# Performance work log

Hardware: AMD Instinct MI355X
Metric: run time of the kernel (lower is better)

The kernel has to match this reference:

```python
import jax, jax.numpy as jnp
import numpy as np

N, IN, HID, OUT = 8192, 512, 256, 128

def setup_inputs() -> dict:
    key = jax.random.key(0)
    k1, k2, k3, k4 = jax.random.split(key, 4)
    adj = jax.random.uniform(k1, (N, N), dtype=jnp.float32)
    feature = jax.random.normal(k2, (N, IN), dtype=jnp.float32)
    W1 = jax.random.normal(k3, (IN, HID), dtype=jnp.float32) * (1.0 / np.sqrt(IN))
    b1 = jnp.zeros((HID,), dtype=jnp.float32)
    W2 = jax.random.normal(k4, (HID, OUT), dtype=jnp.float32) * (1.0 / np.sqrt(HID))
    b2 = jnp.zeros((OUT,), dtype=jnp.float32)
    return {"adj": adj, "feature": feature, "W1": W1, "b1": b1, "W2": W2, "b2": b2}

def reference(adj, feature, W1, b1, W2, b2):
    # GCN encoder: layer1 (relu) then layer2 (linear output)
    h = jax.nn.relu(adj @ (feature @ W1) + b1)   # [N, HID]
    h = adj @ (h @ W2) + b2                      # [N, OUT]
    # InnerProductDecoder: sigmoid(flatten(h @ h.T))
    logits = h @ h.T                             # [N, N]
    h_noise = jax.nn.sigmoid(logits.reshape(-1)) # [N*N]
    return (h_noise, h)
```

## Files before the change

### kernel.cpp

```cpp
#include <hip/hip_runtime.h>


typedef __bf16 bf16x8_t __attribute__((ext_vector_type(8)));
typedef __bf16 bf16x4_t __attribute__((ext_vector_type(4)));
typedef float  f32x4_t  __attribute__((ext_vector_type(4)));

#define MFMA_BF16(a, b, c) __builtin_amdgcn_mfma_f32_16x16x32_bf16((a), (b), (c), 0, 0, 0)

__device__ __forceinline__ bf16x8_t cvt8(float4 u, float4 v) {
    bf16x8_t o;
    o[0] = (__bf16)u.x; o[1] = (__bf16)u.y; o[2] = (__bf16)u.z; o[3] = (__bf16)u.w;
    o[4] = (__bf16)v.x; o[5] = (__bf16)v.y; o[6] = (__bf16)v.z; o[7] = (__bf16)v.w;
    return o;
}

template<int AUX>
__device__ __forceinline__ void gload_lds16(const float* g, float* l) {
    __builtin_amdgcn_global_load_lds(
        (const __attribute__((address_space(1))) unsigned int*)g,
        (__attribute__((address_space(3))) unsigned int*)l, 16, 0, AUX);
}

__global__ __launch_bounds__(256) void cast_all(
    const float* __restrict__ feat, const float* __restrict__ W1,
    const float* __restrict__ W2, __bf16* __restrict__ fb,
    __bf16* __restrict__ w1t, __bf16* __restrict__ w2t)
{
    const int j = blockIdx.x * 256 + threadIdx.x;
    if (j < 524288) {
        const float4* p = (const float4*)feat + (size_t)j * 2;
        float4 u = p[0], v = p[1];
        *(bf16x8_t*)(fb + (size_t)j * 8) = cvt8(u, v);
    } else if (j < 524288 + 131072) {
        int t = j - 524288;
        int k = t >> 8, n = t & 255;
        w1t[n * 512 + k] = (__bf16)W1[t];
    } else if (j < 524288 + 131072 + 32768) {
        int t = j - 655360;
        int k = t >> 7, n = t & 127;
        w2t[n * 256 + k] = (__bf16)W2[t];
    }
}

template<int MT, int WC>
__global__ __launch_bounds__(256, 2) void gemm_bt_cbf16(
    const __bf16* __restrict__ X, const __bf16* __restrict__ Yb,
    __bf16* __restrict__ C, int K, int N)
{
    constexpr int WR = 4 / WC;
    constexpr int BM = WR * MT * 16;
    constexpr int BN = WC * 64;
    const int mblk = blockIdx.x, nblk = blockIdx.y;
    const int w = threadIdx.x >> 6, lane = threadIdx.x & 63;
    const int wr = w / WC, wc = w % WC;
    const int q = lane >> 4, l16 = lane & 15;
    const int mbase = mblk * BM + wr * (MT * 16);
    const int nbase = nblk * BN + wc * 64;

    f32x4_t acc[MT][4];
    const f32x4_t z = {0.f, 0.f, 0.f, 0.f};
#pragma unroll
    for (int i = 0; i < MT; i++)
#pragma unroll
        for (int jj = 0; jj < 4; jj++) acc[i][jj] = z;

    const __bf16* Xr[MT];
    const __bf16* Yr[4];
#pragma unroll
    for (int i = 0; i < MT; i++) Xr[i] = X + (size_t)(mbase + i * 16 + l16) * K + q * 8;
#pragma unroll
    for (int jj = 0; jj < 4; jj++) Yr[jj] = Yb + (size_t)(nbase + jj * 16 + l16) * K + q * 8;

    for (int k = 0; k < K; k += 32) {
        bf16x8_t a[MT], b[4];
#pragma unroll
        for (int i = 0; i < MT; i++) a[i] = *(const bf16x8_t*)(Xr[i] + k);
#pragma unroll
        for (int jj = 0; jj < 4; jj++) b[jj] = *(const bf16x8_t*)(Yr[jj] + k);
#pragma unroll
        for (int i = 0; i < MT; i++)
#pragma unroll
            for (int jj = 0; jj < 4; jj++) acc[i][jj] = MFMA_BF16(a[i], b[jj], acc[i][jj]);
    }

#pragma unroll
    for (int i = 0; i < MT; i++)
#pragma unroll
        for (int jj = 0; jj < 4; jj++) {
            const int row0 = mbase + i * 16 + q * 4;
            const int col = nbase + jj * 16 + l16;
#pragma unroll
            for (int r = 0; r < 4; r++)
                C[(size_t)(row0 + r) * N + col] = (__bf16)acc[i][jj][r];
        }
}

template<int NN>
__global__ __launch_bounds__(256, 2) void gemm_adj_lds(
    const float* __restrict__ A, const __bf16* __restrict__ Y,
    float* __restrict__ P, int kchunk)
{
    constexpr int NT = NN / 64;
    __shared__ float As[2][4096];

    const int mblk = blockIdx.x;
    const int ks = blockIdx.y;
    const int w = threadIdx.x >> 6, lane = threadIdx.x & 63;
    const int q = lane >> 4, l16 = lane & 15;
    const int kbase = ks * kchunk;
    const int ntiles = kchunk >> 6;

    const int lrow = lane >> 4;
    const int lg = lane & 15;
    const float* gsrc[4];
    int loff[4];
#pragma unroll
    for (int j = 0; j < 4; j++) {
        const int row = j * 16 + w * 4 + lrow;
        const int colswz = ((lg ^ (row & 15)) << 2);
        gsrc[j] = A + (size_t)(mblk * 64 + row) * 8192 + kbase + colswz;
        loff[j] = row * 64 + (lg << 2);
    }

    const __bf16* Yr[NT];
#pragma unroll
    for (int jj = 0; jj < NT; jj++)
        Yr[jj] = Y + (size_t)(w * (NN / 4) + jj * 16 + l16) * 8192 + q * 8;

    f32x4_t acc[4][NT];
    const f32x4_t z = {0.f, 0.f, 0.f, 0.f};
#pragma unroll
    for (int i = 0; i < 4; i++)
#pragma unroll
        for (int jj = 0; jj < NT; jj++) acc[i][jj] = z;

#pragma unroll
    for (int j = 0; j < 4; j++) gload_lds16<2>(gsrc[j], &As[0][0] + loff[j]);

    int buf = 0;
    for (int kt = 0; kt < ntiles; kt++) {
        const int kk = kbase + (kt << 6);

        bf16x8_t breg[2][NT];
#pragma unroll
        for (int s = 0; s < 2; s++)
#pragma unroll
            for (int jj = 0; jj < NT; jj++)
                breg[s][jj] = *(const bf16x8_t*)(Yr[jj] + kk + s * 32);

        __syncthreads();

        if (kt + 1 < ntiles) {
            const int koff = (kt + 1) << 6;
#pragma unroll
            for (int j = 0; j < 4; j++)
                gload_lds16<2>(gsrc[j] + koff, &As[buf ^ 1][0] + loff[j]);
        }

        const float* __restrict__ L = &As[buf][0];
#pragma unroll
        for (int s = 0; s < 2; s++) {
            bf16x8_t a[4];
#pragma unroll
            for (int i = 0; i < 4; i++) {
                const int r = i * 16 + l16;
                const int g0 = ((s * 8 + q * 2) ^ l16) << 2;
                const int g1 = ((s * 8 + q * 2 + 1) ^ l16) << 2;
                float4 u = *(const float4*)(L + r * 64 + g0);
                float4 v = *(const float4*)(L + r * 64 + g1);
                a[i] = cvt8(u, v);
            }
#pragma unroll
            for (int i = 0; i < 4; i++)
#pragma unroll
                for (int jj = 0; jj < NT; jj++)
                    acc[i][jj] = MFMA_BF16(a[i], breg[s][jj], acc[i][jj]);
        }
        buf ^= 1;
    }

#pragma unroll
    for (int i = 0; i < 4; i++)
#pragma unroll
        for (int jj = 0; jj < NT; jj++) {
            const int row0 = mblk * 64 + i * 16 + q * 4;
            const int col = w * (NN / 4) + jj * 16 + l16;
            float* pp = P + ((size_t)ks * 8192 + row0) * NN + col;
#pragma unroll
            for (int r = 0; r < 4; r++) pp[(size_t)r * NN] = acc[i][jj][r];
        }
}

__global__ __launch_bounds__(256) void epi_relu_bias(
    const float* __restrict__ P, const float* __restrict__ bias,
    __bf16* __restrict__ H)
{
    const size_t SL = (size_t)8192 * 256;
    const size_t idx = ((size_t)blockIdx.x * 256 + threadIdx.x) * 4;
    float4 s0 = *(const float4*)(P + idx);
    float4 s1 = *(const float4*)(P + SL + idx);
    float4 s2 = *(const float4*)(P + 2 * SL + idx);
    float4 s3 = *(const float4*)(P + 3 * SL + idx);
    const int col = (int)(idx & 255);
    float4 bb = *(const float4*)(bias + col);
    float r0 = fmaxf(s0.x + s1.x + s2.x + s3.x + bb.x, 0.f);
    float r1 = fmaxf(s0.y + s1.y + s2.y + s3.y + bb.y, 0.f);
    float r2 = fmaxf(s0.z + s1.z + s2.z + s3.z + bb.z, 0.f);
    float r3 = fmaxf(s0.w + s1.w + s2.w + s3.w + bb.w, 0.f);
    bf16x4_t o;
    o[0] = (__bf16)r0; o[1] = (__bf16)r1; o[2] = (__bf16)r2; o[3] = (__bf16)r3;
    *(bf16x4_t*)(H + idx) = o;
}

__global__ __launch_bounds__(256) void epi_bias_out(
    const float* __restrict__ P, const float* __restrict__ bias,
    float* __restrict__ Hout, __bf16* __restrict__ Hbf)
{
    const size_t SL = (size_t)8192 * 128;
    const size_t idx = ((size_t)blockIdx.x * 256 + threadIdx.x) * 4;
    float4 s0 = *(const float4*)(P + idx);
    float4 s1 = *(const float4*)(P + SL + idx);
    float4 s2 = *(const float4*)(P + 2 * SL + idx);
    float4 s3 = *(const float4*)(P + 3 * SL + idx);
    const int col = (int)(idx & 127);
    float4 bb = *(const float4*)(bias + col);
    float4 o;
    o.x = s0.x + s1.x + s2.x + s3.x + bb.x;
    o.y = s0.y + s1.y + s2.y + s3.y + bb.y;
    o.z = s0.z + s1.z + s2.z + s3.z + bb.z;
    o.w = s0.w + s1.w + s2.w + s3.w + bb.w;
    *(float4*)(Hout + idx) = o;
    bf16x4_t ob;
    ob[0] = (__bf16)o.x; ob[1] = (__bf16)o.y; ob[2] = (__bf16)o.z; ob[3] = (__bf16)o.w;
    *(bf16x4_t*)(Hbf + idx) = ob;
}

__global__ __launch_bounds__(256, 2) void gemm_sig(
    const __bf16* __restrict__ H, float* __restrict__ out)
{
    const int mblk = blockIdx.x, nblk = blockIdx.y;
    const int w = threadIdx.x >> 6, lane = threadIdx.x & 63;
    const int wr = w >> 1, wc = w & 1;
    const int q = lane >> 4, l16 = lane & 15;
    const int mbase = mblk * 128 + wr * 64;
    const int nbase = nblk * 128 + wc * 64;

    f32x4_t acc[4][4];
    const f32x4_t z = {0.f, 0.f, 0.f, 0.f};
#pragma unroll
    for (int i = 0; i < 4; i++)
#pragma unroll
        for (int jj = 0; jj < 4; jj++) acc[i][jj] = z;

#pragma unroll
    for (int k = 0; k < 128; k += 32) {
        bf16x8_t a[4], b[4];
#pragma unroll
        for (int i = 0; i < 4; i++)
            a[i] = *(const bf16x8_t*)(H + (size_t)(mbase + i * 16 + l16) * 128 + k + q * 8);
#pragma unroll
        for (int jj = 0; jj < 4; jj++)
            b[jj] = *(const bf16x8_t*)(H + (size_t)(nbase + jj * 16 + l16) * 128 + k + q * 8);
#pragma unroll
        for (int i = 0; i < 4; i++)
#pragma unroll
            for (int jj = 0; jj < 4; jj++) acc[i][jj] = MFMA_BF16(a[i], b[jj], acc[i][jj]);
    }

#pragma unroll
    for (int i = 0; i < 4; i++)
#pragma unroll
        for (int jj = 0; jj < 4; jj++) {
            const int row0 = mbase + i * 16 + q * 4;
            const int col = nbase + jj * 16 + l16;
#pragma unroll
            for (int r = 0; r < 4; r++) {
                float x = acc[i][jj][r];
                out[(size_t)(row0 + r) * 8192 + col] = 1.0f / (1.0f + __expf(-x));
            }
        }
}

extern "C" void kernel_launch(void* const* d_in, const int* in_sizes, int n_in,
                              void* d_out, int out_size, void* d_ws, size_t ws_size,
                              hipStream_t stream)
{
    const float* adj  = (const float*)d_in[0];
    const float* feat = (const float*)d_in[1];
    const float* W1   = (const float*)d_in[2];
    const float* b1   = (const float*)d_in[3];
    const float* W2   = (const float*)d_in[4];
    const float* b2   = (const float*)d_in[5];
    float* out = (float*)d_out;

    char* p = (char*)d_ws;
    __bf16* featbf = (__bf16*)p; p += (size_t)8192 * 512 * 2;
    __bf16* W1T    = (__bf16*)p; p += (size_t)256 * 512 * 2;
    __bf16* W2T    = (__bf16*)p; p += (size_t)128 * 256 * 2;
    __bf16* t1T    = (__bf16*)p; p += (size_t)256 * 8192 * 2;
    __bf16* h1     = (__bf16*)p; p += (size_t)8192 * 256 * 2;
    __bf16* t2T    = (__bf16*)p; p += (size_t)128 * 8192 * 2;
    __bf16* hbf    = (__bf16*)p; p += (size_t)8192 * 128 * 2;
    float* part    = (float*)p;

    cast_all<<<2688, 256, 0, stream>>>(feat, W1, W2, featbf, W1T, W2T);
    gemm_bt_cbf16<2, 2><<<dim3(4, 64), 256, 0, stream>>>(W1T, featbf, t1T, 512, 8192);
    gemm_adj_lds<256><<<dim3(128, 4), 256, 0, stream>>>(adj, t1T, part, 2048);
    epi_relu_bias<<<2048, 256, 0, stream>>>(part, b1, h1);
    gemm_bt_cbf16<2, 2><<<dim3(2, 64), 256, 0, stream>>>(W2T, h1, t2T, 256, 8192);
    gemm_adj_lds<128><<<dim3(128, 4), 256, 0, stream>>>(adj, t2T, part, 2048);
    epi_bias_out<<<1024, 256, 0, stream>>>(part, b2, out + (size_t)8192 * 8192, hbf);
    gemm_sig<<<dim3(64, 64), 256, 0, stream>>>(hbf, out);
}
```

Measured before the change: 625.0 us.

## Pre-cast adjacency to bf16 once and reuse it in both aggregation GEMMs

Adds a kernel that converts the full 8192x8192 fp32 adjacency matrix to bf16 in workspace once. Both adjacency GEMMs then stage bf16 tiles into LDS with a new XOR swizzle and feed the MFMAs directly, with no per-tile fp32-to-bf16 conversion and half the LDS footprint. It also raises the K-split from 4 to 8 and changes the tiling of the second small GEMM. The trade is an extra 256MB read plus 128MB write for the cast, and doubled partial-sum traffic in the epilogues, in exchange for cheaper inner loops and a smaller matrix that may stay in the large last-level cache for the second pass.

```diff
diff --git a/kernel.cpp b/kernel.cpp
--- a/kernel.cpp
+++ b/kernel.cpp
@@ -1,5 +1,7 @@
 #include <hip/hip_runtime.h>
 
+
+#define KSPLIT 8
 
 typedef __bf16 bf16x8_t __attribute__((ext_vector_type(8)));
 typedef __bf16 bf16x4_t __attribute__((ext_vector_type(4)));
@@ -14,11 +16,19 @@
     return o;
 }
 
-template<int AUX>
-__device__ __forceinline__ void gload_lds16(const float* g, float* l) {
+__device__ __forceinline__ void gload_lds16(const void* g, void* l) {
     __builtin_amdgcn_global_load_lds(
         (const __attribute__((address_space(1))) unsigned int*)g,
-        (__attribute__((address_space(3))) unsigned int*)l, 16, 0, AUX);
+        (__attribute__((address_space(3))) unsigned int*)l, 16, 0, 0);
+}
+
+__global__ __launch_bounds__(256) void cast_adj(
+    const float* __restrict__ adj, __bf16* __restrict__ ab)
+{
+    const size_t j = (size_t)blockIdx.x * 256 + threadIdx.x;
+    const float4* p = (const float4*)adj + j * 2;
+    float4 u = p[0], v = p[1];
+    *(bf16x8_t*)(ab + j * 8) = cvt8(u, v);
 }
 
 __global__ __launch_bounds__(256) void cast_all(
@@ -96,12 +106,12 @@
 }
 
 template<int NN>
-__global__ __launch_bounds__(256, 2) void gemm_adj_lds(
-    const float* __restrict__ A, const __bf16* __restrict__ Y,
+__global__ __launch_bounds__(256, 2) void gemm_adj_bf(
+    const __bf16* __restrict__ A, const __bf16* __restrict__ Y,
     float* __restrict__ P, int kchunk)
 {
     constexpr int NT = NN / 64;
-    __shared__ float As[2][4096];
+    __shared__ __bf16 As[2][4096];
 
     const int mblk = blockIdx.x;
     const int ks = blockIdx.y;
@@ -110,16 +120,15 @@
     const int kbase = ks * kchunk;
     const int ntiles = kchunk >> 6;
 
-    const int lrow = lane >> 4;
-    const int lg = lane & 15;
-    const float* gsrc[4];
-    int loff[4];
-#pragma unroll
-    for (int j = 0; j < 4; j++) {
-        const int row = j * 16 + w * 4 + lrow;
-        const int colswz = ((lg ^ (row & 15)) << 2);
-        gsrc[j] = A + (size_t)(mblk * 64 + row) * 8192 + kbase + colswz;
-        loff[j] = row * 64 + (lg << 2);
+    const __bf16* gsrc[2];
+    int loff[2];
+#pragma unroll
+    for (int j = 0; j < 2; j++) {
+        const int row = j * 32 + w * 8 + (lane >> 3);
+        const int gdst = lane & 7;
+        const int gsrcg = gdst ^ (row & 7);
+        gsrc[j] = A + (size_t)(mblk * 64 + row) * 8192 + kbase + gsrcg * 8;
+        loff[j] = row * 64 + gdst * 8;
     }
 
     const __bf16* Yr[NT];
@@ -135,7 +144,7 @@
         for (int jj = 0; jj < NT; jj++) acc[i][jj] = z;
 
 #pragma unroll
-    for (int j = 0; j < 4; j++) gload_lds16<2>(gsrc[j], &As[0][0] + loff[j]);
+    for (int j = 0; j < 2; j++) gload_lds16(gsrc[j], &As[0][0] + loff[j]);
 
     int buf = 0;
     for (int kt = 0; kt < ntiles; kt++) {
@@ -153,22 +162,19 @@
         if (kt + 1 < ntiles) {
             const int koff = (kt + 1) << 6;
 #pragma unroll
-            for (int j = 0; j < 4; j++)
-                gload_lds16<2>(gsrc[j] + koff, &As[buf ^ 1][0] + loff[j]);
-        }
-
-        const float* __restrict__ L = &As[buf][0];
+            for (int j = 0; j < 2; j++)
+                gload_lds16(gsrc[j] + koff, &As[buf ^ 1][0] + loff[j]);
+        }
+
+        const __bf16* __restrict__ L = &As[buf][0];
 #pragma unroll
         for (int s = 0; s < 2; s++) {
             bf16x8_t a[4];
 #pragma unroll
             for (int i = 0; i < 4; i++) {
                 const int r = i * 16 + l16;
-                const int g0 = ((s * 8 + q * 2) ^ l16) << 2;
-                const int g1 = ((s * 8 + q * 2 + 1) ^ l16) << 2;
-                float4 u = *(const float4*)(L + r * 64 + g0);
-                float4 v = *(const float4*)(L + r * 64 + g1);
-                a[i] = cvt8(u, v);
+                const int g = ((s * 4 + q) ^ (r & 7)) * 8;
+                a[i] = *(const bf16x8_t*)(L + r * 64 + g);
             }
 #pragma unroll
             for (int i = 0; i < 4; i++)
@@ -197,18 +203,20 @@
 {
     const size_t SL = (size_t)8192 * 256;
     const size_t idx = ((size_t)blockIdx.x * 256 + threadIdx.x) * 4;
-    float4 s0 = *(const float4*)(P + idx);
-    float4 s1 = *(const float4*)(P + SL + idx);
-    float4 s2 = *(const float4*)(P + 2 * SL + idx);
-    float4 s3 = *(const float4*)(P + 3 * SL + idx);
+    float4 s;
+    s.x = s.y = s.z = s.w = 0.f;
+#pragma unroll
+    for (int k = 0; k < KSPLIT; k++) {
+        float4 t = *(const float4*)(P + k * SL + idx);
+        s.x += t.x; s.y += t.y; s.z += t.z; s.w += t.w;
+    }
     const int col = (int)(idx & 255);
     float4 bb = *(const float4*)(bias + col);
-    float r0 = fmaxf(s0.x + s1.x + s2.x + s3.x + bb.x, 0.f);
-    float r1 = fmaxf(s0.y + s1.y + s2.y + s3.y + bb.y, 0.f);
-    float r2 = fmaxf(s0.z + s1.z + s2.z + s3.z + bb.z, 0.f);
-    float r3 = fmaxf(s0.w + s1.w + s2.w + s3.w + bb.w, 0.f);
     bf16x4_t o;
-    o[0] = (__bf16)r0; o[1] = (__bf16)r1; o[2] = (__bf16)r2; o[3] = (__bf16)r3;
+    o[0] = (__bf16)fmaxf(s.x + bb.x, 0.f);
+    o[1] = (__bf16)fmaxf(s.y + bb.y, 0.f);
+    o[2] = (__bf16)fmaxf(s.z + bb.z, 0.f);
+    o[3] = (__bf16)fmaxf(s.w + bb.w, 0.f);
     *(bf16x4_t*)(H + idx) = o;
 }
 
@@ -218,17 +226,17 @@
 {
     const size_t SL = (size_t)8192 * 128;
     const size_t idx = ((size_t)blockIdx.x * 256 + threadIdx.x) * 4;
-    float4 s0 = *(const float4*)(P + idx);
-    float4 s1 = *(const float4*)(P + SL + idx);
-    float4 s2 = *(const float4*)(P + 2 * SL + idx);
-    float4 s3 = *(const float4*)(P + 3 * SL + idx);
+    float4 s;
+    s.x = s.y = s.z = s.w = 0.f;
+#pragma unroll
+    for (int k = 0; k < KSPLIT; k++) {
+        float4 t = *(const float4*)(P + k * SL + idx);
+        s.x += t.x; s.y += t.y; s.z += t.z; s.w += t.w;
+    }
     const int col = (int)(idx & 127);
     float4 bb = *(const float4*)(bias + col);
     float4 o;
-    o.x = s0.x + s1.x + s2.x + s3.x + bb.x;
-    o.y = s0.y + s1.y + s2.y + s3.y + bb.y;
-    o.z = s0.z + s1.z + s2.z + s3.z + bb.z;
-    o.w = s0.w + s1.w + s2.w + s3.w + bb.w;
+    o.x = s.x + bb.x; o.y = s.y + bb.y; o.z = s.z + bb.z; o.w = s.w + bb.w;
     *(float4*)(Hout + idx) = o;
     bf16x4_t ob;
     ob[0] = (__bf16)o.x; ob[1] = (__bf16)o.y; ob[2] = (__bf16)o.z; ob[3] = (__bf16)o.w;
@@ -294,6 +302,7 @@
     float* out = (float*)d_out;
 
     char* p = (char*)d_ws;
+    __bf16* adjbf  = (__bf16*)p; p += (size_t)8192 * 8192 * 2;
     __bf16* featbf = (__bf16*)p; p += (size_t)8192 * 512 * 2;
     __bf16* W1T    = (__bf16*)p; p += (size_t)256 * 512 * 2;
     __bf16* W2T    = (__bf16*)p; p += (size_t)128 * 256 * 2;
@@ -303,12 +312,13 @@
     __bf16* hbf    = (__bf16*)p; p += (size_t)8192 * 128 * 2;
     float* part    = (float*)p;
 
+    cast_adj<<<32768, 256, 0, stream>>>(adj, adjbf);
     cast_all<<<2688, 256, 0, stream>>>(feat, W1, W2, featbf, W1T, W2T);
     gemm_bt_cbf16<2, 2><<<dim3(4, 64), 256, 0, stream>>>(W1T, featbf, t1T, 512, 8192);
-    gemm_adj_lds<256><<<dim3(128, 4), 256, 0, stream>>>(adj, t1T, part, 2048);
+    gemm_adj_bf<256><<<dim3(128, KSPLIT), 256, 0, stream>>>(adjbf, t1T, part, 8192 / KSPLIT);
     epi_relu_bias<<<2048, 256, 0, stream>>>(part, b1, h1);
-    gemm_bt_cbf16<2, 2><<<dim3(2, 64), 256, 0, stream>>>(W2T, h1, t2T, 256, 8192);
-    gemm_adj_lds<128><<<dim3(128, 4), 256, 0, stream>>>(adj, t2T, part, 2048);
+    gemm_bt_cbf16<1, 2><<<dim3(4, 64), 256, 0, stream>>>(W2T, h1, t2T, 256, 8192);
+    gemm_adj_bf<128><<<dim3(128, KSPLIT), 256, 0, stream>>>(adjbf, t2T, part, 8192 / KSPLIT);
     epi_bias_out<<<1024, 256, 0, stream>>>(part, b2, out + (size_t)8192 * 8192, hbf);
     gemm_sig<<<dim3(64, 64), 256, 0, stream>>>(hbf, out);
 }
```

Result: slower. 691.2 us (+10.6%).
